# Kernel optimization log

Measured on AMD Instinct MI355X. Metric: run time of the kernel, lower is better.

Reference implementation:

```python
import jax, jax.numpy as jnp
import numpy as np

EMBED = 512
HEADS = 64
DK = EMBED // HEADS  # == n_wires_attn == 8
NW_FFN = 8
FFN = 2048
EPS = 1e-5


def _layernorm(x, g, b):
    mu = jnp.mean(x, axis=-1, keepdims=True)
    var = jnp.var(x, axis=-1, keepdims=True)
    return (x - mu) * jax.lax.rsqrt(var + EPS) * g + b


def setup_inputs() -> dict:
    key = jax.random.key(0)
    ks = jax.random.split(key, 12)
    d = {
        "x": jax.random.normal(ks[0], (4, 1024, EMBED), dtype=jnp.float32),
        # attention quantum RX params (one per wire, shared across heads/tokens)
        "phi": jax.random.normal(ks[1], (DK,), dtype=jnp.float32) * 0.1,
        # combine_heads linear
        "Wc": jax.random.normal(ks[2], (EMBED, EMBED), dtype=jnp.float32) / np.sqrt(EMBED),
        "bc": jnp.zeros((EMBED,), dtype=jnp.float32),
        # FFN quantum RY params
        "theta": jax.random.normal(ks[3], (NW_FFN,), dtype=jnp.float32) * 0.1,
        "W1": jax.random.normal(ks[4], (NW_FFN, FFN), dtype=jnp.float32) / np.sqrt(NW_FFN),
        "b1": jnp.zeros((FFN,), dtype=jnp.float32),
        "W2": jax.random.normal(ks[5], (FFN, EMBED), dtype=jnp.float32) / np.sqrt(FFN),
        "b2": jnp.zeros((EMBED,), dtype=jnp.float32),
        "g1": jnp.ones((EMBED,), dtype=jnp.float32),
        "be1": jnp.zeros((EMBED,), dtype=jnp.float32),
        "g2": jnp.ones((EMBED,), dtype=jnp.float32),
        "be2": jnp.zeros((EMBED,), dtype=jnp.float32),
    }
    return d


def reference(x, phi, Wc, bc, theta, W1, b1, W2, b2, g1, be1, g2, be2):
    B, S, E = x.shape
    # --- quantum attention projections ---
    # Per head-row of DK features: RX(x_i) encoder then trainable RX(phi_i),
    xh = x.reshape(B, S, HEADS, DK)
    qkv = jnp.cos(xh + phi)                     # [B,S,H,DK]
    qkv = jnp.transpose(qkv, (0, 2, 1, 3))      # [B,H,S,DK]
    scores = jnp.einsum('bhqd,bhkd->bhqk', qkv, qkv) / jnp.sqrt(jnp.float32(DK))
    attn = jax.nn.softmax(scores, axis=-1)
    out = jnp.einsum('bhqk,bhkd->bhqd', attn, qkv)
    out = jnp.transpose(out, (0, 2, 1, 3)).reshape(B, S, E)
    attn_out = out @ Wc.T if False else out @ Wc + bc  # combine_heads linear
    x1 = _layernorm(x + attn_out, g1, be1)
    # --- quantum FFN: RX(x_i) then trainable RY(theta_i) -> <Z> = cos(x_i)*cos(theta_i)
    qout = jnp.cos(x1[..., :NW_FFN]) * jnp.cos(theta)   # [B,S,NW_FFN]
    h = jax.nn.relu(qout @ W1 + b1)
    ffn_out = h @ W2 + b2
    return _layernorm(x1 + ffn_out, g2, be2)
```

## Files before the change

kernel.cpp:

```cpp
#include <hip/hip_runtime.h>
#include <hip/hip_bf16.h>
#include <math.h>

#define B 4
#define S 1024
#define E 512
#define H 64
#define DK 8
#define FFN 2048
#define BS (B*S)

#define CSCALE 0.7141879f

#if __has_builtin(__builtin_amdgcn_exp2f)
#define EXP2F(x) __builtin_amdgcn_exp2f(x)
#else
#define EXP2F(x) exp2f(x)
#endif

typedef __attribute__((ext_vector_type(8))) short short8;
typedef __attribute__((ext_vector_type(4))) float float4a;

union U8 { short8 v; unsigned u[4]; };
union F4 { float4a v; float f[4]; };

__device__ __forceinline__ unsigned short f2bf(float f) {
    unsigned u = __builtin_bit_cast(unsigned, f);
    u = (u + 0x7fffu + ((u >> 16) & 1u)) >> 16;
    return (unsigned short)u;
}
__device__ __forceinline__ float bf2f(unsigned short h) {
    return __builtin_bit_cast(float, (unsigned)h << 16);
}
__device__ __forceinline__ unsigned packbf(float a, float b) {
    return __builtin_amdgcn_perm(__builtin_bit_cast(unsigned, a),
                                 __builtin_bit_cast(unsigned, b), 0x07060302u);
}
__device__ __forceinline__ unsigned packbf_rn(float a, float b) {
    return ((unsigned)f2bf(a) << 16) | f2bf(b);
}
__device__ __forceinline__ int pidx(int k) {
    return (k & ~31) | (((k >> 2) & 3) << 3) | (((k >> 4) & 1) << 2) | (k & 3);
}

__device__ __forceinline__ void glds16(const void* g, void* l) {
    __builtin_amdgcn_global_load_lds(
        (const __attribute__((address_space(1))) void*)g,
        (__attribute__((address_space(3))) void*)l, 16, 0, 0);
}

__global__ __launch_bounds__(512) void attn_conv_kernel(const float* __restrict__ x,
                                                        const float* __restrict__ phi,
                                                        const float* __restrict__ Wc,
                                                        const float* __restrict__ W2,
                                                        const float* __restrict__ W1,
                                                        const float* __restrict__ b1,
                                                        unsigned short* __restrict__ Afrag,
                                                        unsigned short* __restrict__ W2f,
                                                        unsigned short* __restrict__ Wcf,
                                                        unsigned short* __restrict__ W1f) {
    __shared__ unsigned short kv[(S + 16) * DK];
    __shared__ unsigned short vtp[9][S + 8];
    int bid = blockIdx.x;
    int tid = threadIdx.x;
    const short8 z8 = {0,0,0,0,0,0,0,0};

    if (bid < 336) {
        int idx = bid * 512 + tid;
        if (idx < 131072) {
            int lane = idx & 63, c = idx >> 6;
            int ntile = c >> 6, kb32 = c & 63;
            int g = lane >> 4, col = lane & 15;
            int n = ntile * 16 + col, kb = kb32 * 32;
            short8 o;
            #pragma unroll
            for (int j = 0; j < 8; j++) {
                int k = kb + 16 * (j >> 2) + 4 * g + (j & 3);
                o[j] = (short)f2bf(W2[(size_t)k * 512 + n]);
            }
            *(short8*)&W2f[(size_t)idx * 8] = o;
        } else if (idx < 163840) {
            int i2 = idx - 131072;
            int lane = i2 & 63, c = i2 >> 6;
            int ntile = c >> 4, kb32 = c & 15;
            int g = lane >> 4, col = lane & 15;
            int n = ntile * 16 + col, kb = kb32 * 32;
            short8 o;
            #pragma unroll
            for (int j = 0; j < 8; j++)
                o[j] = (short)f2bf(Wc[(size_t)(kb + g * 8 + j) * 512 + n]);
            *(short8*)&Wcf[(size_t)i2 * 8] = o;
        } else {
            int i3 = idx - 163840;
            if (i3 < 2048) {
                short8 o;
                #pragma unroll
                for (int j = 0; j < 8; j++) o[j] = (short)f2bf(W1[j * FFN + i3]);
                *(short8*)&W1f[(size_t)i3 * 8] = o;
            } else if (i3 < 4096) {
                int f = i3 - 2048;
                short8 o = z8;
                o[0] = (short)f2bf(b1[f]);
                *(short8*)&W1f[(size_t)i3 * 8] = o;
            } else if (i3 < 4112) {
                *(short8*)&W1f[(size_t)i3 * 8] = z8;
            }
        }
        return;
    }

    int abid = bid - 336;
    int head = abid >> 2, qquad = abid & 3;
    int b = head >> 6, hh = head & 63;

    float ph[DK];
    #pragma unroll
    for (int d = 0; d < DK; d++) ph[d] = phi[d];

    {
        int r2 = tid * 2;
        unsigned short vb[8][2];
        #pragma unroll
        for (int j = 0; j < 2; j++) {
            const float* xp = x + ((size_t)(b * S + r2 + j)) * E + hh * DK;
            float4 u = *(const float4*)xp;
            float4 v = *(const float4*)(xp + 4);
            float c[8] = {__cosf(u.x+ph[0]), __cosf(u.y+ph[1]), __cosf(u.z+ph[2]), __cosf(u.w+ph[3]),
                          __cosf(v.x+ph[4]), __cosf(v.y+ph[5]), __cosf(v.z+ph[6]), __cosf(v.w+ph[7])};
            U8 kr;
            kr.u[0] = packbf_rn(c[1] * CSCALE, c[0] * CSCALE);
            kr.u[1] = packbf_rn(c[3] * CSCALE, c[2] * CSCALE);
            kr.u[2] = packbf_rn(c[5] * CSCALE, c[4] * CSCALE);
            kr.u[3] = packbf_rn(c[7] * CSCALE, c[6] * CSCALE);
            *(short8*)&kv[(r2 + j) * DK] = kr.v;
            #pragma unroll
            for (int d = 0; d < 8; d++) vb[d][j] = f2bf(c[d]);
        }
        int pr = pidx(r2);
        #pragma unroll
        for (int d = 0; d < 8; d++)
            *(unsigned*)&vtp[d][pr] = (unsigned)vb[d][0] | ((unsigned)vb[d][1] << 16);
        *(unsigned*)&vtp[8][pr] = 0x3F803F80u;
    }
    if (tid < 16) *(short8*)&kv[(S + tid) * DK] = z8;
    __syncthreads();

    int w = tid >> 6, lane = tid & 63, col = lane & 15, g = lane >> 4;
    bool g0 = (g == 0);
    int q0 = qquad * 256 + w * 32;
    const float4a zc = {0.f,0.f,0.f,0.f};

    short8 aq[2];
    #pragma unroll
    for (int t = 0; t < 2; t++)
        aq[t] = g0 ? *(const short8*)&kv[(q0 + t*16 + col) * DK] : z8;

    float4a acc[2];
    acc[0] = zc; acc[1] = zc;

    int vrow = col < 8 ? col : 8;
    const unsigned short* vbase = &vtp[vrow][0];

    int off0 = g0 ? col * DK : S * DK;
    int off1 = g0 ? (16 + col) * DK : S * DK;
    int stepo = g0 ? 32 * DK : 0;

    short8 bk0 = *(const short8*)&kv[off0];
    short8 bk1 = *(const short8*)&kv[off1];
    off0 += stepo; off1 += stepo;
    short8 bkN0 = *(const short8*)&kv[off0];
    short8 bkN1 = *(const short8*)&kv[off1];
    off0 += stepo; off1 += stepo;
    float4a s00 = __builtin_amdgcn_mfma_f32_16x16x32_bf16(bk0, aq[0], zc, 0,0,0);
    float4a s01 = __builtin_amdgcn_mfma_f32_16x16x32_bf16(bk1, aq[0], zc, 0,0,0);
    float4a s10 = __builtin_amdgcn_mfma_f32_16x16x32_bf16(bk0, aq[1], zc, 0,0,0);
    float4a s11 = __builtin_amdgcn_mfma_f32_16x16x32_bf16(bk1, aq[1], zc, 0,0,0);
    short8 vf = *(const short8*)(vbase + g * 8);

#define EXP_PACK(PF0, PF1)                                                      \
        F4 S00, S01, S10, S11;                                                  \
        S00.v = s00; S01.v = s01; S10.v = s10; S11.v = s11;                     \
        float ea0 = EXP2F(S00.f[0]);                                            \
        float ea1 = EXP2F(S00.f[1]);                                            \
        float ea2 = EXP2F(S00.f[2]);                                            \
        float ea3 = EXP2F(S00.f[3]);                                            \
        float eb0 = EXP2F(S01.f[0]);                                            \
        float eb1 = EXP2F(S01.f[1]);                                            \
        float eb2 = EXP2F(S01.f[2]);                                            \
        float eb3 = EXP2F(S01.f[3]);                                            \
        float ec0 = EXP2F(S10.f[0]);                                            \
        float ec1 = EXP2F(S10.f[1]);                                            \
        float ec2 = EXP2F(S10.f[2]);                                            \
        float ec3 = EXP2F(S10.f[3]);                                            \
        float ed0 = EXP2F(S11.f[0]);                                            \
        float ed1 = EXP2F(S11.f[1]);                                            \
        float ed2 = EXP2F(S11.f[2]);                                            \
        float ed3 = EXP2F(S11.f[3]);                                            \
        PF0.u[0] = packbf(ea1, ea0);                                            \
        PF0.u[1] = packbf(ea3, ea2);                                            \
        PF0.u[2] = packbf(eb1, eb0);                                            \
        PF0.u[3] = packbf(eb3, eb2);                                            \
        PF1.u[0] = packbf(ec1, ec0);                                            \
        PF1.u[1] = packbf(ec3, ec2);                                            \
        PF1.u[2] = packbf(ed1, ed0);                                            \
        PF1.u[3] = packbf(ed3, ed2);

    for (int kb = 0; kb < S - 32; kb += 32) {
        short8 nb0 = *(const short8*)&kv[off0];
        short8 nb1 = *(const short8*)&kv[off1];
        off0 += stepo; off1 += stepo;
        short8 vfN = *(const short8*)(vbase + kb + 32 + g * 8);
        U8 pf0, pf1;
        { EXP_PACK(pf0, pf1) }
        float4a t00 = __builtin_amdgcn_mfma_f32_16x16x32_bf16(bkN0, aq[0], zc, 0,0,0);
        float4a t01 = __builtin_amdgcn_mfma_f32_16x16x32_bf16(bkN1, aq[0], zc, 0,0,0);
        float4a t10 = __builtin_amdgcn_mfma_f32_16x16x32_bf16(bkN0, aq[1], zc, 0,0,0);
        float4a t11 = __builtin_amdgcn_mfma_f32_16x16x32_bf16(bkN1, aq[1], zc, 0,0,0);
        acc[0] = __builtin_amdgcn_mfma_f32_16x16x32_bf16(vf, pf0.v, acc[0], 0,0,0);
        acc[1] = __builtin_amdgcn_mfma_f32_16x16x32_bf16(vf, pf1.v, acc[1], 0,0,0);
        s00 = t00; s01 = t01; s10 = t10; s11 = t11;
        bkN0 = nb0; bkN1 = nb1; vf = vfN;
    }
    {
        U8 pf0, pf1;
        { EXP_PACK(pf0, pf1) }
        acc[0] = __builtin_amdgcn_mfma_f32_16x16x32_bf16(vf, pf0.v, acc[0], 0,0,0);
        acc[1] = __builtin_amdgcn_mfma_f32_16x16x32_bf16(vf, pf1.v, acc[1], 0,0,0);
    }
#undef EXP_PACK

    int lp8 = ((hh & 3) * 16 + col) * 8;
    #pragma unroll
    for (int t = 0; t < 2; t++) {
        F4 a; a.v = acc[t];
        float denom = __shfl(a.f[0], 32 + col);
        float inv = __builtin_amdgcn_rcpf(denom);
        if (g < 2) {
            int chunk = (hh >> 2) * 256 + (b * 64 + qquad * 16 + w * 2 + t);
            uint2 o;
            o.x = packbf_rn(a.f[1] * inv, a.f[0] * inv);
            o.y = packbf_rn(a.f[3] * inv, a.f[2] * inv);
            *(uint2*)&Afrag[(size_t)chunk * 512 + lp8 + g * 4] = o;
        }
    }
}

__global__ __launch_bounds__(512) void combine_ln1(const unsigned short* __restrict__ Afrag,
                                                   const unsigned short* __restrict__ Wcf,
                                                   const float* __restrict__ bc,
                                                   const float* __restrict__ x,
                                                   const float* __restrict__ g1,
                                                   const float* __restrict__ be1,
                                                   float* __restrict__ x1out,
                                                   unsigned short* __restrict__ qoutbf,
                                                   const float* __restrict__ theta) {
    __shared__ unsigned short As[16 * 64 * 8];
    __shared__ float xout[16][516];
    int tt = blockIdx.x;
    int tid = threadIdx.x;
    int w = tid >> 6, lane = tid & 63;
    int wbase = (tid & ~63) * 8;

    #pragma unroll
    for (int r = 0; r < 2; r++) {
        const unsigned short* gsrc =
            Afrag + ((size_t)((r * 8 + w) * 256 + tt) * 64 + lane) * 8;
        glds16(gsrc, &As[r * 4096 + wbase]);
    }
    asm volatile("s_waitcnt vmcnt(0)" ::: "memory");
    __syncthreads();

    int col = lane & 15, g = lane >> 4;
    const float4a zc = {0.f,0.f,0.f,0.f};
    float4a acc[4];
    #pragma unroll
    for (int nt = 0; nt < 4; nt++) acc[nt] = zc;

    const unsigned short* wp = Wcf + ((size_t)(w * 4096) + lane) * 8;

    short8 bfA[4], bfB[4];
    #pragma unroll
    for (int nt = 0; nt < 4; nt++)
        bfA[nt] = *(const short8*)(wp + nt * 8192);

    for (int kb32 = 0; kb32 < 16; kb32 += 2) {
        #pragma unroll
        for (int nt = 0; nt < 4; nt++)
            bfB[nt] = *(const short8*)(wp + nt * 8192 + (kb32 + 1) * 512);
        short8 af = *(const short8*)&As[(kb32 * 64 + lane) * 8];
        #pragma unroll
        for (int nt = 0; nt < 4; nt++)
            acc[nt] = __builtin_amdgcn_mfma_f32_16x16x32_bf16(af, bfA[nt], acc[nt], 0, 0, 0);
        if (kb32 + 2 < 16) {
            #pragma unroll
            for (int nt = 0; nt < 4; nt++)
                bfA[nt] = *(const short8*)(wp + nt * 8192 + (kb32 + 2) * 512);
        }
        af = *(const short8*)&As[((kb32 + 1) * 64 + lane) * 8];
        #pragma unroll
        for (int nt = 0; nt < 4; nt++)
            acc[nt] = __builtin_amdgcn_mfma_f32_16x16x32_bf16(af, bfB[nt], acc[nt], 0, 0, 0);
    }
    #pragma unroll
    for (int nt = 0; nt < 4; nt++) {
        int n = w * 64 + nt * 16 + col;
        float bb = bc[n];
        #pragma unroll
        for (int r = 0; r < 4; r++)
            xout[g * 4 + r][n] = acc[nt][r] + bb;
    }
    __syncthreads();

    int hl = lane >> 5, l = lane & 31;
    int token = w * 2 + hl;
    int e0 = l * 16;
    size_t grow = ((size_t)tt * 16 + token) * 512;
    float v[16];
    float s = 0.f, sq = 0.f;
    #pragma unroll
    for (int u = 0; u < 4; u++) {
        float4 xv = *(const float4*)&x[grow + e0 + u * 4];
        float4 pv = *(const float4*)&xout[token][e0 + u * 4];
        float a0 = xv.x + pv.x, a1 = xv.y + pv.y, a2 = xv.z + pv.z, a3 = xv.w + pv.w;
        v[u*4] = a0; v[u*4+1] = a1; v[u*4+2] = a2; v[u*4+3] = a3;
        s += a0 + a1 + a2 + a3;
        sq += a0*a0 + a1*a1 + a2*a2 + a3*a3;
    }
    #pragma unroll
    for (int off = 1; off <= 16; off <<= 1) {
        s  += __shfl_xor(s, off);
        sq += __shfl_xor(sq, off);
    }
    float mu = s * (1.f / 512.f);
    float var = sq * (1.f / 512.f) - mu * mu;
    float rstd = rsqrtf(var + 1e-5f);
    float y[16];
    #pragma unroll
    for (int u = 0; u < 4; u++) {
        float4 gv = *(const float4*)&g1[e0 + u * 4];
        float4 bv = *(const float4*)&be1[e0 + u * 4];
        y[u*4]   = (v[u*4]   - mu) * rstd * gv.x + bv.x;
        y[u*4+1] = (v[u*4+1] - mu) * rstd * gv.y + bv.y;
        y[u*4+2] = (v[u*4+2] - mu) * rstd * gv.z + bv.z;
        y[u*4+3] = (v[u*4+3] - mu) * rstd * gv.w + bv.w;
        float4 o = make_float4(y[u*4], y[u*4+1], y[u*4+2], y[u*4+3]);
        *(float4*)&x1out[grow + e0 + u * 4] = o;
    }
    if (l == 0) {
        U8 q;
        q.u[0] = packbf_rn(__cosf(y[1]) * __cosf(theta[1]), __cosf(y[0]) * __cosf(theta[0]));
        q.u[1] = packbf_rn(__cosf(y[3]) * __cosf(theta[3]), __cosf(y[2]) * __cosf(theta[2]));
        q.u[2] = packbf_rn(__cosf(y[5]) * __cosf(theta[5]), __cosf(y[4]) * __cosf(theta[4]));
        q.u[3] = packbf_rn(__cosf(y[7]) * __cosf(theta[7]), __cosf(y[6]) * __cosf(theta[6]));
        *(short8*)&qoutbf[((size_t)tt * 16 + token) * 8] = q.v;
    }
}

__global__ __launch_bounds__(256) void ffn_mfma(const unsigned short* __restrict__ qbf,
                                                const unsigned short* __restrict__ W1fg,
                                                const unsigned short* __restrict__ W2f,
                                                const float* __restrict__ b2,
                                                unsigned short* __restrict__ Cbf) {
    __shared__ float accs[2][64][36];
    int tid = threadIdx.x;
    int w = tid >> 6, lane = tid & 63, col = lane & 15, g = lane >> 4;
    int ngw = w & 1, kh = w >> 1;
    int tb = blockIdx.x >> 2, nb = blockIdx.x & 3;
    int mw = tb * 32;
    int ntile0 = nb * 8 + ngw * 4;
    int kb32b = kh * 32;
    const short8 z8 = {0,0,0,0,0,0,0,0};
    const short8 one8 = {(short)0x3F80,0,0,0,0,0,0,0};
    const float4a zc = {0.f,0.f,0.f,0.f};

    short8 qf[2];
    #pragma unroll
    for (int t = 0; t < 2; t++)
        qf[t] = (g == 0) ? *(const short8*)&qbf[(size_t)(mw + t * 16 + col) * 8]
                         : (g == 1 ? one8 : z8);

    float4a acc[2][4];
    #pragma unroll
    for (int t = 0; t < 2; t++)
        #pragma unroll
        for (int nt = 0; nt < 4; nt++) acc[t][nt] = zc;

    const unsigned short* w2p = W2f + (size_t)ntile0 * 64 * 512 + lane * 8;
    const unsigned short* w1p =
        (g == 0) ? W1fg + (size_t)(kb32b * 32 + col) * 8 :
        (g == 1) ? W1fg + 16384 + (size_t)(kb32b * 32 + col) * 8 :
                   W1fg + 32768;
    int w1step = (g < 2) ? 256 : 0;

    short8 afA[4], afB[4], w1A0, w1A1, w1B0, w1B1;
    #pragma unroll
    for (int nt = 0; nt < 4; nt++)
        afA[nt] = *(const short8*)(w2p + nt * 32768 + (size_t)kb32b * 512);
    w1A0 = *(const short8*)w1p;
    w1A1 = *(const short8*)(w1p + 128);
    w1p += w1step;

#define FFN_BODY(AF, W10, W11)                                                    \
    {                                                                             \
        _Pragma("unroll")                                                         \
        for (int t = 0; t < 2; t++) {                                             \
            float4a h0 = __builtin_amdgcn_mfma_f32_16x16x32_bf16(W10, qf[t], zc, 0,0,0); \
            float4a h1 = __builtin_amdgcn_mfma_f32_16x16x32_bf16(W11, qf[t], zc, 0,0,0); \
            F4 H0, H1; H0.v = h0; H1.v = h1;                                      \
            float e00 = fmaxf(H0.f[0], 0.f);                                      \
            float e01 = fmaxf(H0.f[1], 0.f);                                      \
            float e02 = fmaxf(H0.f[2], 0.f);                                      \
            float e03 = fmaxf(H0.f[3], 0.f);                                      \
            float e10 = fmaxf(H1.f[0], 0.f);                                      \
            float e11 = fmaxf(H1.f[1], 0.f);                                      \
            float e12 = fmaxf(H1.f[2], 0.f);                                      \
            float e13 = fmaxf(H1.f[3], 0.f);                                      \
            U8 pf;                                                                \
            pf.u[0] = packbf(e01, e00);                                           \
            pf.u[1] = packbf(e03, e02);                                           \
            pf.u[2] = packbf(e11, e10);                                           \
            pf.u[3] = packbf(e13, e12);                                           \
            _Pragma("unroll")                                                     \
            for (int nt = 0; nt < 4; nt++)                                        \
                acc[t][nt] = __builtin_amdgcn_mfma_f32_16x16x32_bf16(AF[nt], pf.v, \
                                                                     acc[t][nt], 0,0,0); \
        }                                                                         \
    }

    for (int i = 0; i < 32; i += 2) {
        int kb32 = kb32b + i;
        #pragma unroll
        for (int nt = 0; nt < 4; nt++)
            afB[nt] = *(const short8*)(w2p + nt * 32768 + (size_t)(kb32 + 1) * 512);
        w1B0 = *(const short8*)w1p;
        w1B1 = *(const short8*)(w1p + 128);
        w1p += w1step;
        FFN_BODY(afA, w1A0, w1A1)
        #pragma unroll
        for (int nt = 0; nt < 4; nt++)
            afA[nt] = *(const short8*)(w2p + nt * 32768 + (size_t)(kb32 + 2) * 512);
        w1A0 = *(const short8*)w1p;
        w1A1 = *(const short8*)(w1p + 128);
        w1p += w1step;
        FFN_BODY(afB, w1B0, w1B1)
    }
#undef FFN_BODY

    if (kh == 1) {
        #pragma unroll
        for (int t = 0; t < 2; t++)
            #pragma unroll
            for (int nt = 0; nt < 4; nt++)
                *(float4a*)&accs[ngw][lane][(t * 4 + nt) * 4] = acc[t][nt];
    }
    __syncthreads();
    if (kh == 0) {
        #pragma unroll
        for (int t = 0; t < 2; t++)
            #pragma unroll
            for (int nt = 0; nt < 4; nt++)
                acc[t][nt] = acc[t][nt] +
                    *(const float4a*)&accs[ngw][lane][(t * 4 + nt) * 4];
        int n0 = ntile0 * 16;
        #pragma unroll
        for (int nt = 0; nt < 4; nt++) {
            float4 bb = *(const float4*)&b2[n0 + nt * 16 + 4 * g];
            #pragma unroll
            for (int t = 0; t < 2; t++) {
                F4 a; a.v = acc[t][nt];
                uint2 o;
                o.x = packbf_rn(a.f[1] + bb.y, a.f[0] + bb.x);
                o.y = packbf_rn(a.f[3] + bb.w, a.f[2] + bb.z);
                *(uint2*)&Cbf[(size_t)(mw + t * 16 + col) * 512 + n0 + nt * 16 + 4 * g] = o;
            }
        }
    }
}

__global__ __launch_bounds__(256) void ln_kernel(const float* __restrict__ a,
                                                 const unsigned short* __restrict__ r,
                                                 const float* __restrict__ g,
                                                 const float* __restrict__ be,
                                                 float* __restrict__ out) {
    int t = blockIdx.x * 4 + (threadIdx.x >> 6);
    int lane = threadIdx.x & 63;
    size_t base = (size_t)t * E;
    int e0 = lane * 8;
    float4 a0 = *(const float4*)&a[base + e0];
    float4 a1 = *(const float4*)&a[base + e0 + 4];
    uint4 rv = *(const uint4*)&r[base + e0];
    float v[8];
    v[0] = a0.x + bf2f((unsigned short)(rv.x & 0xffff));
    v[1] = a0.y + bf2f((unsigned short)(rv.x >> 16));
    v[2] = a0.z + bf2f((unsigned short)(rv.y & 0xffff));
    v[3] = a0.w + bf2f((unsigned short)(rv.y >> 16));
    v[4] = a1.x + bf2f((unsigned short)(rv.z & 0xffff));
    v[5] = a1.y + bf2f((unsigned short)(rv.z >> 16));
    v[6] = a1.z + bf2f((unsigned short)(rv.w & 0xffff));
    v[7] = a1.w + bf2f((unsigned short)(rv.w >> 16));
    float s = 0.f, sq = 0.f;
    #pragma unroll
    for (int i = 0; i < 8; i++) { s += v[i]; sq += v[i] * v[i]; }
    #pragma unroll
    for (int off = 1; off <= 32; off <<= 1) {
        s  += __shfl_xor(s, off);
        sq += __shfl_xor(sq, off);
    }
    float mu = s * (1.f / E);
    float var = sq * (1.f / E) - mu * mu;
    float rstd = rsqrtf(var + 1e-5f);
    float4 g0 = *(const float4*)&g[e0];
    float4 g1v = *(const float4*)&g[e0 + 4];
    float4 b0 = *(const float4*)&be[e0];
    float4 b1v = *(const float4*)&be[e0 + 4];
    float4 o0, o1;
    o0.x = (v[0] - mu) * rstd * g0.x + b0.x;
    o0.y = (v[1] - mu) * rstd * g0.y + b0.y;
    o0.z = (v[2] - mu) * rstd * g0.z + b0.z;
    o0.w = (v[3] - mu) * rstd * g0.w + b0.w;
    o1.x = (v[4] - mu) * rstd * g1v.x + b1v.x;
    o1.y = (v[5] - mu) * rstd * g1v.y + b1v.y;
    o1.z = (v[6] - mu) * rstd * g1v.z + b1v.z;
    o1.w = (v[7] - mu) * rstd * g1v.w + b1v.w;
    *(float4*)&out[base + e0] = o0;
    *(float4*)&out[base + e0 + 4] = o1;
}

extern "C" void kernel_launch(void* const* d_in, const int* in_sizes, int n_in,
                              void* d_out, int out_size, void* d_ws, size_t ws_size,
                              hipStream_t stream) {
    const float* x     = (const float*)d_in[0];
    const float* phi   = (const float*)d_in[1];
    const float* Wc    = (const float*)d_in[2];
    const float* bc    = (const float*)d_in[3];
    const float* theta = (const float*)d_in[4];
    const float* W1    = (const float*)d_in[5];
    const float* b1    = (const float*)d_in[6];
    const float* W2    = (const float*)d_in[7];
    const float* b2    = (const float*)d_in[8];
    const float* g1    = (const float*)d_in[9];
    const float* be1   = (const float*)d_in[10];
    const float* g2    = (const float*)d_in[11];
    const float* be2   = (const float*)d_in[12];
    float* out = (float*)d_out;

    float* ws = (float*)d_ws;
    unsigned short* Afrag  = (unsigned short*)ws;
    unsigned short* W2f    = (unsigned short*)(ws + 1048576);
    unsigned short* Wcf    = (unsigned short*)(ws + 1572864);
    unsigned short* W1f    = (unsigned short*)(ws + 1703936);
    unsigned short* qoutbf = (unsigned short*)(ws + 1736704);

    attn_conv_kernel<<<1360, 512, 0, stream>>>(x, phi, Wc, W2, W1, b1,
                                               Afrag, W2f, Wcf, W1f);
    combine_ln1<<<256, 512, 0, stream>>>(Afrag, Wcf, bc, x, g1, be1,
                                         out, qoutbf, theta);
    ffn_mfma<<<512, 256, 0, stream>>>(qoutbf, W1f, W2f, b2, Afrag);
    ln_kernel<<<1024, 256, 0, stream>>>(out, Afrag, g2, be2, out);
}
```

Measured before the change: 156.9 us.

## Fuse combine, FFN and final layernorm into one persistent kernel with grid barriers

Merges the combine+LN1, FFN MFMA and LN2 kernels into a single 256-block kernel that uses a software grid barrier (atomic counter plus generation) between phases. The aim is to drop two kernel launches and their launch gaps. The counter is reset by the first kernel. The barrier relies on all 256 blocks being co-resident, and the FFN phase now runs with 256 blocks of 512 threads in place of 512 blocks of 256. The FFN output buffer Cbf aliases Afrag, which phase one reads; this is safe only because the grid barrier orders the two phases.

```diff
diff --git a/kernel.cpp b/kernel.cpp
--- a/kernel.cpp
+++ b/kernel.cpp
@@ -47,6 +47,25 @@
     __builtin_amdgcn_global_load_lds(
         (const __attribute__((address_space(1))) void*)g,
         (__attribute__((address_space(3))) void*)l, 16, 0, 0);
+}
+
+__device__ __forceinline__ void gridbar(unsigned* cnt, unsigned* gen) {
+    __syncthreads();
+    __threadfence();
+    if (threadIdx.x == 0) {
+        unsigned g = __hip_atomic_load(gen, __ATOMIC_RELAXED, __HIP_MEMORY_SCOPE_AGENT);
+        unsigned old = __hip_atomic_fetch_add(cnt, 1u, __ATOMIC_ACQ_REL,
+                                              __HIP_MEMORY_SCOPE_AGENT);
+        if (old == 255u) {
+            __hip_atomic_store(cnt, 0u, __ATOMIC_RELAXED, __HIP_MEMORY_SCOPE_AGENT);
+            __hip_atomic_store(gen, g + 1u, __ATOMIC_RELEASE, __HIP_MEMORY_SCOPE_AGENT);
+        } else {
+            while (__hip_atomic_load(gen, __ATOMIC_ACQUIRE,
+                                     __HIP_MEMORY_SCOPE_AGENT) == g)
+                __builtin_amdgcn_s_sleep(2);
+        }
+    }
+    __syncthreads();
 }
 
 __global__ __launch_bounds__(512) void attn_conv_kernel(const float* __restrict__ x,
@@ -58,7 +77,8 @@
                                                         unsigned short* __restrict__ Afrag,
                                                         unsigned short* __restrict__ W2f,
                                                         unsigned short* __restrict__ Wcf,
-                                                        unsigned short* __restrict__ W1f) {
+                                                        unsigned short* __restrict__ W1f,
+                                                        unsigned* __restrict__ bar) {
     __shared__ unsigned short kv[(S + 16) * DK];
     __shared__ unsigned short vtp[9][S + 8];
     int bid = blockIdx.x;
@@ -67,6 +87,7 @@
 
     if (bid < 336) {
         int idx = bid * 512 + tid;
+        if (idx == 0) { bar[0] = 0u; bar[1] = 0u; }
         if (idx < 131072) {
             int lane = idx & 63, c = idx >> 6;
             int ntile = c >> 6, kb32 = c & 63;
@@ -245,285 +266,290 @@
     }
 }
 
-__global__ __launch_bounds__(512) void combine_ln1(const unsigned short* __restrict__ Afrag,
-                                                   const unsigned short* __restrict__ Wcf,
-                                                   const float* __restrict__ bc,
-                                                   const float* __restrict__ x,
-                                                   const float* __restrict__ g1,
-                                                   const float* __restrict__ be1,
-                                                   float* __restrict__ x1out,
-                                                   unsigned short* __restrict__ qoutbf,
-                                                   const float* __restrict__ theta) {
-    __shared__ unsigned short As[16 * 64 * 8];
-    __shared__ float xout[16][516];
-    int tt = blockIdx.x;
-    int tid = threadIdx.x;
-    int w = tid >> 6, lane = tid & 63;
-    int wbase = (tid & ~63) * 8;
-
-    #pragma unroll
-    for (int r = 0; r < 2; r++) {
-        const unsigned short* gsrc =
-            Afrag + ((size_t)((r * 8 + w) * 256 + tt) * 64 + lane) * 8;
-        glds16(gsrc, &As[r * 4096 + wbase]);
-    }
-    asm volatile("s_waitcnt vmcnt(0)" ::: "memory");
-    __syncthreads();
-
-    int col = lane & 15, g = lane >> 4;
-    const float4a zc = {0.f,0.f,0.f,0.f};
-    float4a acc[4];
-    #pragma unroll
-    for (int nt = 0; nt < 4; nt++) acc[nt] = zc;
-
-    const unsigned short* wp = Wcf + ((size_t)(w * 4096) + lane) * 8;
-
-    short8 bfA[4], bfB[4];
-    #pragma unroll
-    for (int nt = 0; nt < 4; nt++)
-        bfA[nt] = *(const short8*)(wp + nt * 8192);
-
-    for (int kb32 = 0; kb32 < 16; kb32 += 2) {
-        #pragma unroll
-        for (int nt = 0; nt < 4; nt++)
-            bfB[nt] = *(const short8*)(wp + nt * 8192 + (kb32 + 1) * 512);
-        short8 af = *(const short8*)&As[(kb32 * 64 + lane) * 8];
-        #pragma unroll
-        for (int nt = 0; nt < 4; nt++)
-            acc[nt] = __builtin_amdgcn_mfma_f32_16x16x32_bf16(af, bfA[nt], acc[nt], 0, 0, 0);
-        if (kb32 + 2 < 16) {
-            #pragma unroll
-            for (int nt = 0; nt < 4; nt++)
-                bfA[nt] = *(const short8*)(wp + nt * 8192 + (kb32 + 2) * 512);
-        }
-        af = *(const short8*)&As[((kb32 + 1) * 64 + lane) * 8];
-        #pragma unroll
-        for (int nt = 0; nt < 4; nt++)
-            acc[nt] = __builtin_amdgcn_mfma_f32_16x16x32_bf16(af, bfB[nt], acc[nt], 0, 0, 0);
-    }
-    #pragma unroll
-    for (int nt = 0; nt < 4; nt++) {
-        int n = w * 64 + nt * 16 + col;
-        float bb = bc[n];
-        #pragma unroll
-        for (int r = 0; r < 4; r++)
-            xout[g * 4 + r][n] = acc[nt][r] + bb;
-    }
-    __syncthreads();
-
-    int hl = lane >> 5, l = lane & 31;
-    int token = w * 2 + hl;
-    int e0 = l * 16;
-    size_t grow = ((size_t)tt * 16 + token) * 512;
-    float v[16];
-    float s = 0.f, sq = 0.f;
-    #pragma unroll
-    for (int u = 0; u < 4; u++) {
-        float4 xv = *(const float4*)&x[grow + e0 + u * 4];
-        float4 pv = *(const float4*)&xout[token][e0 + u * 4];
-        float a0 = xv.x + pv.x, a1 = xv.y + pv.y, a2 = xv.z + pv.z, a3 = xv.w + pv.w;
-        v[u*4] = a0; v[u*4+1] = a1; v[u*4+2] = a2; v[u*4+3] = a3;
-        s += a0 + a1 + a2 + a3;
-        sq += a0*a0 + a1*a1 + a2*a2 + a3*a3;
-    }
-    #pragma unroll
-    for (int off = 1; off <= 16; off <<= 1) {
-        s  += __shfl_xor(s, off);
-        sq += __shfl_xor(sq, off);
-    }
-    float mu = s * (1.f / 512.f);
-    float var = sq * (1.f / 512.f) - mu * mu;
-    float rstd = rsqrtf(var + 1e-5f);
-    float y[16];
-    #pragma unroll
-    for (int u = 0; u < 4; u++) {
-        float4 gv = *(const float4*)&g1[e0 + u * 4];
-        float4 bv = *(const float4*)&be1[e0 + u * 4];
-        y[u*4]   = (v[u*4]   - mu) * rstd * gv.x + bv.x;
-        y[u*4+1] = (v[u*4+1] - mu) * rstd * gv.y + bv.y;
-        y[u*4+2] = (v[u*4+2] - mu) * rstd * gv.z + bv.z;
-        y[u*4+3] = (v[u*4+3] - mu) * rstd * gv.w + bv.w;
-        float4 o = make_float4(y[u*4], y[u*4+1], y[u*4+2], y[u*4+3]);
-        *(float4*)&x1out[grow + e0 + u * 4] = o;
-    }
-    if (l == 0) {
-        U8 q;
-        q.u[0] = packbf_rn(__cosf(y[1]) * __cosf(theta[1]), __cosf(y[0]) * __cosf(theta[0]));
-        q.u[1] = packbf_rn(__cosf(y[3]) * __cosf(theta[3]), __cosf(y[2]) * __cosf(theta[2]));
-        q.u[2] = packbf_rn(__cosf(y[5]) * __cosf(theta[5]), __cosf(y[4]) * __cosf(theta[4]));
-        q.u[3] = packbf_rn(__cosf(y[7]) * __cosf(theta[7]), __cosf(y[6]) * __cosf(theta[6]));
-        *(short8*)&qoutbf[((size_t)tt * 16 + token) * 8] = q.v;
-    }
-}
-
-__global__ __launch_bounds__(256) void ffn_mfma(const unsigned short* __restrict__ qbf,
-                                                const unsigned short* __restrict__ W1fg,
-                                                const unsigned short* __restrict__ W2f,
-                                                const float* __restrict__ b2,
-                                                unsigned short* __restrict__ Cbf) {
-    __shared__ float accs[2][64][36];
+__global__ __launch_bounds__(512) void fused_tail(const unsigned short* __restrict__ Afrag,
+                                                  const unsigned short* __restrict__ Wcf,
+                                                  const float* __restrict__ bc,
+                                                  const float* __restrict__ x,
+                                                  const float* __restrict__ g1,
+                                                  const float* __restrict__ be1,
+                                                  const float* __restrict__ theta,
+                                                  const unsigned short* __restrict__ W1fg,
+                                                  const unsigned short* __restrict__ W2f,
+                                                  const float* __restrict__ b2,
+                                                  const float* __restrict__ g2,
+                                                  const float* __restrict__ be2,
+                                                  unsigned short* __restrict__ qoutbf,
+                                                  float* __restrict__ out,
+                                                  unsigned short* __restrict__ Cbf,
+                                                  unsigned* __restrict__ bar) {
+    __shared__ union {
+        struct { unsigned short As[16 * 64 * 8]; float xout[16][516]; } a;
+        struct { float accs[2][2][64][36]; } b3;
+    } sm;
+    int bid = blockIdx.x;
     int tid = threadIdx.x;
     int w = tid >> 6, lane = tid & 63, col = lane & 15, g = lane >> 4;
-    int ngw = w & 1, kh = w >> 1;
-    int tb = blockIdx.x >> 2, nb = blockIdx.x & 3;
-    int mw = tb * 32;
-    int ntile0 = nb * 8 + ngw * 4;
-    int kb32b = kh * 32;
+    const float4a zc = {0.f,0.f,0.f,0.f};
     const short8 z8 = {0,0,0,0,0,0,0,0};
-    const short8 one8 = {(short)0x3F80,0,0,0,0,0,0,0};
-    const float4a zc = {0.f,0.f,0.f,0.f};
-
-    short8 qf[2];
-    #pragma unroll
-    for (int t = 0; t < 2; t++)
-        qf[t] = (g == 0) ? *(const short8*)&qbf[(size_t)(mw + t * 16 + col) * 8]
-                         : (g == 1 ? one8 : z8);
-
-    float4a acc[2][4];
-    #pragma unroll
-    for (int t = 0; t < 2; t++)
-        #pragma unroll
-        for (int nt = 0; nt < 4; nt++) acc[t][nt] = zc;
-
-    const unsigned short* w2p = W2f + (size_t)ntile0 * 64 * 512 + lane * 8;
-    const unsigned short* w1p =
-        (g == 0) ? W1fg + (size_t)(kb32b * 32 + col) * 8 :
-        (g == 1) ? W1fg + 16384 + (size_t)(kb32b * 32 + col) * 8 :
-                   W1fg + 32768;
-    int w1step = (g < 2) ? 256 : 0;
-
-    short8 afA[4], afB[4], w1A0, w1A1, w1B0, w1B1;
-    #pragma unroll
-    for (int nt = 0; nt < 4; nt++)
-        afA[nt] = *(const short8*)(w2p + nt * 32768 + (size_t)kb32b * 512);
-    w1A0 = *(const short8*)w1p;
-    w1A1 = *(const short8*)(w1p + 128);
-    w1p += w1step;
-
-#define FFN_BODY(AF, W10, W11)                                                    \
-    {                                                                             \
-        _Pragma("unroll")                                                         \
-        for (int t = 0; t < 2; t++) {                                             \
-            float4a h0 = __builtin_amdgcn_mfma_f32_16x16x32_bf16(W10, qf[t], zc, 0,0,0); \
-            float4a h1 = __builtin_amdgcn_mfma_f32_16x16x32_bf16(W11, qf[t], zc, 0,0,0); \
-            F4 H0, H1; H0.v = h0; H1.v = h1;                                      \
-            float e00 = fmaxf(H0.f[0], 0.f);                                      \
-            float e01 = fmaxf(H0.f[1], 0.f);                                      \
-            float e02 = fmaxf(H0.f[2], 0.f);                                      \
-            float e03 = fmaxf(H0.f[3], 0.f);                                      \
-            float e10 = fmaxf(H1.f[0], 0.f);                                      \
-            float e11 = fmaxf(H1.f[1], 0.f);                                      \
-            float e12 = fmaxf(H1.f[2], 0.f);                                      \
-            float e13 = fmaxf(H1.f[3], 0.f);                                      \
-            U8 pf;                                                                \
-            pf.u[0] = packbf(e01, e00);                                           \
-            pf.u[1] = packbf(e03, e02);                                           \
-            pf.u[2] = packbf(e11, e10);                                           \
-            pf.u[3] = packbf(e13, e12);                                           \
-            _Pragma("unroll")                                                     \
-            for (int nt = 0; nt < 4; nt++)                                        \
-                acc[t][nt] = __builtin_amdgcn_mfma_f32_16x16x32_bf16(AF[nt], pf.v, \
-                                                                     acc[t][nt], 0,0,0); \
-        }                                                                         \
-    }
-
-    for (int i = 0; i < 32; i += 2) {
-        int kb32 = kb32b + i;
+
+    {
+        int tt = bid;
+        int wbase = (tid & ~63) * 8;
+        #pragma unroll
+        for (int r = 0; r < 2; r++) {
+            const unsigned short* gsrc =
+                Afrag + ((size_t)((r * 8 + w) * 256 + tt) * 64 + lane) * 8;
+            glds16(gsrc, &sm.a.As[r * 4096 + wbase]);
+        }
+        asm volatile("s_waitcnt vmcnt(0)" ::: "memory");
+        __syncthreads();
+
+        float4a acc[4];
+        #pragma unroll
+        for (int nt = 0; nt < 4; nt++) acc[nt] = zc;
+
+        const unsigned short* wp = Wcf + ((size_t)(w * 4096) + lane) * 8;
+
+        short8 bfA[4], bfB[4];
         #pragma unroll
         for (int nt = 0; nt < 4; nt++)
-            afB[nt] = *(const short8*)(w2p + nt * 32768 + (size_t)(kb32 + 1) * 512);
-        w1B0 = *(const short8*)w1p;
-        w1B1 = *(const short8*)(w1p + 128);
-        w1p += w1step;
-        FFN_BODY(afA, w1A0, w1A1)
+            bfA[nt] = *(const short8*)(wp + nt * 8192);
+
+        for (int kb32 = 0; kb32 < 16; kb32 += 2) {
+            #pragma unroll
+            for (int nt = 0; nt < 4; nt++)
+                bfB[nt] = *(const short8*)(wp + nt * 8192 + (kb32 + 1) * 512);
+            short8 af = *(const short8*)&sm.a.As[(kb32 * 64 + lane) * 8];
+            #pragma unroll
+            for (int nt = 0; nt < 4; nt++)
+                acc[nt] = __builtin_amdgcn_mfma_f32_16x16x32_bf16(af, bfA[nt], acc[nt], 0, 0, 0);
+            if (kb32 + 2 < 16) {
+                #pragma unroll
+                for (int nt = 0; nt < 4; nt++)
+                    bfA[nt] = *(const short8*)(wp + nt * 8192 + (kb32 + 2) * 512);
+            }
+            af = *(const short8*)&sm.a.As[((kb32 + 1) * 64 + lane) * 8];
+            #pragma unroll
+            for (int nt = 0; nt < 4; nt++)
+                acc[nt] = __builtin_amdgcn_mfma_f32_16x16x32_bf16(af, bfB[nt], acc[nt], 0, 0, 0);
+        }
+        #pragma unroll
+        for (int nt = 0; nt < 4; nt++) {
+            int n = w * 64 + nt * 16 + col;
+            float bb = bc[n];
+            #pragma unroll
+            for (int r = 0; r < 4; r++)
+                sm.a.xout[g * 4 + r][n] = acc[nt][r] + bb;
+        }
+        __syncthreads();
+
+        int hl = lane >> 5, l = lane & 31;
+        int token = w * 2 + hl;
+        int e0 = l * 16;
+        size_t grow = ((size_t)tt * 16 + token) * 512;
+        float v[16];
+        float s = 0.f, sq = 0.f;
+        #pragma unroll
+        for (int u = 0; u < 4; u++) {
+            float4 xv = *(const float4*)&x[grow + e0 + u * 4];
+            float4 pv = *(const float4*)&sm.a.xout[token][e0 + u * 4];
+            float a0 = xv.x + pv.x, a1 = xv.y + pv.y, a2 = xv.z + pv.z, a3 = xv.w + pv.w;
+            v[u*4] = a0; v[u*4+1] = a1; v[u*4+2] = a2; v[u*4+3] = a3;
+            s += a0 + a1 + a2 + a3;
+            sq += a0*a0 + a1*a1 + a2*a2 + a3*a3;
+        }
+        #pragma unroll
+        for (int off = 1; off <= 16; off <<= 1) {
+            s  += __shfl_xor(s, off);
+            sq += __shfl_xor(sq, off);
+        }
+        float mu = s * (1.f / 512.f);
+        float var = sq * (1.f / 512.f) - mu * mu;
+        float rstd = rsqrtf(var + 1e-5f);
+        float y[16];
+        #pragma unroll
+        for (int u = 0; u < 4; u++) {
+            float4 gv = *(const float4*)&g1[e0 + u * 4];
+            float4 bv = *(const float4*)&be1[e0 + u * 4];
+            y[u*4]   = (v[u*4]   - mu) * rstd * gv.x + bv.x;
+            y[u*4+1] = (v[u*4+1] - mu) * rstd * gv.y + bv.y;
+            y[u*4+2] = (v[u*4+2] - mu) * rstd * gv.z + bv.z;
+            y[u*4+3] = (v[u*4+3] - mu) * rstd * gv.w + bv.w;
+            float4 o = make_float4(y[u*4], y[u*4+1], y[u*4+2], y[u*4+3]);
+            *(float4*)&out[grow + e0 + u * 4] = o;
+        }
+        if (l == 0) {
+            U8 q;
+            q.u[0] = packbf_rn(__cosf(y[1]) * __cosf(theta[1]), __cosf(y[0]) * __cosf(theta[0]));
+            q.u[1] = packbf_rn(__cosf(y[3]) * __cosf(theta[3]), __cosf(y[2]) * __cosf(theta[2]));
+            q.u[2] = packbf_rn(__cosf(y[5]) * __cosf(theta[5]), __cosf(y[4]) * __cosf(theta[4]));
+            q.u[3] = packbf_rn(__cosf(y[7]) * __cosf(theta[7]), __cosf(y[6]) * __cosf(theta[6]));
+            *(short8*)&qoutbf[((size_t)tt * 16 + token) * 8] = q.v;
+        }
+    }
+
+    gridbar(&bar[0], &bar[1]);
+
+    {
+        int sub = w >> 2, lw = w & 3;
+        int fbid = bid * 2 + sub;
+        int ngw = lw & 1, kh = lw >> 1;
+        int tb = fbid >> 2, nb3 = fbid & 3;
+        int mw = tb * 32;
+        int ntile0 = nb3 * 8 + ngw * 4;
+        int kb32b = kh * 32;
+        const short8 one8 = {(short)0x3F80,0,0,0,0,0,0,0};
+
+        short8 qf[2];
+        #pragma unroll
+        for (int t = 0; t < 2; t++)
+            qf[t] = (g == 0) ? *(const short8*)&qoutbf[(size_t)(mw + t * 16 + col) * 8]
+                             : (g == 1 ? one8 : z8);
+
+        float4a acc[2][4];
+        #pragma unroll
+        for (int t = 0; t < 2; t++)
+            #pragma unroll
+            for (int nt = 0; nt < 4; nt++) acc[t][nt] = zc;
+
+        const unsigned short* w2p = W2f + (size_t)ntile0 * 64 * 512 + lane * 8;
+        const unsigned short* w1p =
+            (g == 0) ? W1fg + (size_t)(kb32b * 32 + col) * 8 :
+            (g == 1) ? W1fg + 16384 + (size_t)(kb32b * 32 + col) * 8 :
+                       W1fg + 32768;
+        int w1step = (g < 2) ? 256 : 0;
+
+        short8 afA[4], afB[4], w1A0, w1A1, w1B0, w1B1;
         #pragma unroll
         for (int nt = 0; nt < 4; nt++)
-            afA[nt] = *(const short8*)(w2p + nt * 32768 + (size_t)(kb32 + 2) * 512);
+            afA[nt] = *(const short8*)(w2p + nt * 32768 + (size_t)kb32b * 512);
         w1A0 = *(const short8*)w1p;
         w1A1 = *(const short8*)(w1p + 128);
         w1p += w1step;
-        FFN_BODY(afB, w1B0, w1B1)
-    }
+
+#define FFN_BODY(AF, W10, W11)                                                    \
+        {                                                                         \
+            _Pragma("unroll")                                                     \
+            for (int t = 0; t < 2; t++) {                                         \
+                float4a h0 = __builtin_amdgcn_mfma_f32_16x16x32_bf16(W10, qf[t], zc, 0,0,0); \
+                float4a h1 = __builtin_amdgcn_mfma_f32_16x16x32_bf16(W11, qf[t], zc, 0,0,0); \
+                F4 H0, H1; H0.v = h0; H1.v = h1;                                  \
+                float e00 = fmaxf(H0.f[0], 0.f);                                  \
+                float e01 = fmaxf(H0.f[1], 0.f);                                  \
+                float e02 = fmaxf(H0.f[2], 0.f);                                  \
+                float e03 = fmaxf(H0.f[3], 0.f);                                  \
+                float e10 = fmaxf(H1.f[0], 0.f);                                  \
+                float e11 = fmaxf(H1.f[1], 0.f);                                  \
+                float e12 = fmaxf(H1.f[2], 0.f);                                  \
+                float e13 = fmaxf(H1.f[3], 0.f);                                  \
+                U8 pf;                                                            \
+                pf.u[0] = packbf(e01, e00);                                       \
+                pf.u[1] = packbf(e03, e02);                                       \
+                pf.u[2] = packbf(e11, e10);                                       \
+                pf.u[3] = packbf(e13, e12);                                       \
+                _Pragma("unroll")                                                 \
+                for (int nt = 0; nt < 4; nt++)                                    \
+                    acc[t][nt] = __builtin_amdgcn_mfma_f32_16x16x32_bf16(AF[nt], pf.v, \
+                                                                         acc[t][nt], 0,0,0); \
+            }                                                                     \
+        }
+
+        for (int i = 0; i < 32; i += 2) {
+            int kb32 = kb32b + i;
+            #pragma unroll
+            for (int nt = 0; nt < 4; nt++)
+                afB[nt] = *(const short8*)(w2p + nt * 32768 + (size_t)(kb32 + 1) * 512);
+            w1B0 = *(const short8*)w1p;
+            w1B1 = *(const short8*)(w1p + 128);
+            w1p += w1step;
+            FFN_BODY(afA, w1A0, w1A1)
+            #pragma unroll
+            for (int nt = 0; nt < 4; nt++)
+                afA[nt] = *(const short8*)(w2p + nt * 32768 + (size_t)(kb32 + 2) * 512);
+            w1A0 = *(const short8*)w1p;
+            w1A1 = *(const short8*)(w1p + 128);
+            w1p += w1step;
+            FFN_BODY(afB, w1B0, w1B1)
+        }
 #undef FFN_BODY
 
-    if (kh == 1) {
-        #pragma unroll
-        for (int t = 0; t < 2; t++)
-            #pragma unroll
-            for (int nt = 0; nt < 4; nt++)
-                *(float4a*)&accs[ngw][lane][(t * 4 + nt) * 4] = acc[t][nt];
-    }
-    __syncthreads();
-    if (kh == 0) {
-        #pragma unroll
-        for (int t = 0; t < 2; t++)
-            #pragma unroll
-            for (int nt = 0; nt < 4; nt++)
-                acc[t][nt] = acc[t][nt] +
-                    *(const float4a*)&accs[ngw][lane][(t * 4 + nt) * 4];
-        int n0 = ntile0 * 16;
-        #pragma unroll
-        for (int nt = 0; nt < 4; nt++) {
-            float4 bb = *(const float4*)&b2[n0 + nt * 16 + 4 * g];
-            #pragma unroll
-            for (int t = 0; t < 2; t++) {
-                F4 a; a.v = acc[t][nt];
-                uint2 o;
-                o.x = packbf_rn(a.f[1] + bb.y, a.f[0] + bb.x);
-                o.y = packbf_rn(a.f[3] + bb.w, a.f[2] + bb.z);
-                *(uint2*)&Cbf[(size_t)(mw + t * 16 + col) * 512 + n0 + nt * 16 + 4 * g] = o;
+        if (kh == 1) {
+            #pragma unroll
+            for (int t = 0; t < 2; t++)
+                #pragma unroll
+                for (int nt = 0; nt < 4; nt++)
+                    *(float4a*)&sm.b3.accs[sub][ngw][lane][(t * 4 + nt) * 4] = acc[t][nt];
+        }
+        __syncthreads();
+        if (kh == 0) {
+            #pragma unroll
+            for (int t = 0; t < 2; t++)
+                #pragma unroll
+                for (int nt = 0; nt < 4; nt++)
+                    acc[t][nt] = acc[t][nt] +
+                        *(const float4a*)&sm.b3.accs[sub][ngw][lane][(t * 4 + nt) * 4];
+            int n0 = ntile0 * 16;
+            #pragma unroll
+            for (int nt = 0; nt < 4; nt++) {
+                float4 bb = *(const float4*)&b2[n0 + nt * 16 + 4 * g];
+                #pragma unroll
+                for (int t = 0; t < 2; t++) {
+                    F4 a; a.v = acc[t][nt];
+                    uint2 o;
+                    o.x = packbf_rn(a.f[1] + bb.y, a.f[0] + bb.x);
+                    o.y = packbf_rn(a.f[3] + bb.w, a.f[2] + bb.z);
+                    *(uint2*)&Cbf[(size_t)(mw + t * 16 + col) * 512 + n0 + nt * 16 + 4 * g] = o;
+                }
             }
         }
     }
-}
-
-__global__ __launch_bounds__(256) void ln_kernel(const float* __restrict__ a,
-                                                 const unsigned short* __restrict__ r,
-                                                 const float* __restrict__ g,
-                                                 const float* __restrict__ be,
-                                                 float* __restrict__ out) {
-    int t = blockIdx.x * 4 + (threadIdx.x >> 6);
-    int lane = threadIdx.x & 63;
-    size_t base = (size_t)t * E;
-    int e0 = lane * 8;
-    float4 a0 = *(const float4*)&a[base + e0];
-    float4 a1 = *(const float4*)&a[base + e0 + 4];
-    uint4 rv = *(const uint4*)&r[base + e0];
-    float v[8];
-    v[0] = a0.x + bf2f((unsigned short)(rv.x & 0xffff));
-    v[1] = a0.y + bf2f((unsigned short)(rv.x >> 16));
-    v[2] = a0.z + bf2f((unsigned short)(rv.y & 0xffff));
-    v[3] = a0.w + bf2f((unsigned short)(rv.y >> 16));
-    v[4] = a1.x + bf2f((unsigned short)(rv.z & 0xffff));
-    v[5] = a1.y + bf2f((unsigned short)(rv.z >> 16));
-    v[6] = a1.z + bf2f((unsigned short)(rv.w & 0xffff));
-    v[7] = a1.w + bf2f((unsigned short)(rv.w >> 16));
-    float s = 0.f, sq = 0.f;
+
+    gridbar(&bar[0], &bar[1]);
+
     #pragma unroll
-    for (int i = 0; i < 8; i++) { s += v[i]; sq += v[i] * v[i]; }
-    #pragma unroll
-    for (int off = 1; off <= 32; off <<= 1) {
-        s  += __shfl_xor(s, off);
-        sq += __shfl_xor(sq, off);
-    }
-    float mu = s * (1.f / E);
-    float var = sq * (1.f / E) - mu * mu;
-    float rstd = rsqrtf(var + 1e-5f);
-    float4 g0 = *(const float4*)&g[e0];
-    float4 g1v = *(const float4*)&g[e0 + 4];
-    float4 b0 = *(const float4*)&be[e0];
-    float4 b1v = *(const float4*)&be[e0 + 4];
-    float4 o0, o1;
-    o0.x = (v[0] - mu) * rstd * g0.x + b0.x;
-    o0.y = (v[1] - mu) * rstd * g0.y + b0.y;
-    o0.z = (v[2] - mu) * rstd * g0.z + b0.z;
-    o0.w = (v[3] - mu) * rstd * g0.w + b0.w;
-    o1.x = (v[4] - mu) * rstd * g1v.x + b1v.x;
-    o1.y = (v[5] - mu) * rstd * g1v.y + b1v.y;
-    o1.z = (v[6] - mu) * rstd * g1v.z + b1v.z;
-    o1.w = (v[7] - mu) * rstd * g1v.w + b1v.w;
-    *(float4*)&out[base + e0] = o0;
-    *(float4*)&out[base + e0 + 4] = o1;
+    for (int it = 0; it < 2; it++) {
+        int t = bid * 16 + it * 8 + w;
+        size_t base = (size_t)t * E;
+        int e0 = lane * 8;
+        float4 a0 = *(const float4*)&out[base + e0];
+        float4 a1 = *(const float4*)&out[base + e0 + 4];
+        uint4 rv = *(const uint4*)&Cbf[base + e0];
+        float v[8];
+        v[0] = a0.x + bf2f((unsigned short)(rv.x & 0xffff));
+        v[1] = a0.y + bf2f((unsigned short)(rv.x >> 16));
+        v[2] = a0.z + bf2f((unsigned short)(rv.y & 0xffff));
+        v[3] = a0.w + bf2f((unsigned short)(rv.y >> 16));
+        v[4] = a1.x + bf2f((unsigned short)(rv.z & 0xffff));
+        v[5] = a1.y + bf2f((unsigned short)(rv.z >> 16));
+        v[6] = a1.z + bf2f((unsigned short)(rv.w & 0xffff));
+        v[7] = a1.w + bf2f((unsigned short)(rv.w >> 16));
+        float s = 0.f, sq = 0.f;
+        #pragma unroll
+        for (int i = 0; i < 8; i++) { s += v[i]; sq += v[i] * v[i]; }
+        #pragma unroll
+        for (int off = 1; off <= 32; off <<= 1) {
+            s  += __shfl_xor(s, off);
+            sq += __shfl_xor(sq, off);
+        }
+        float mu = s * (1.f / E);
+        float var = sq * (1.f / E) - mu * mu;
+        float rstd = rsqrtf(var + 1e-5f);
+        float4 g0v = *(const float4*)&g2[e0];
+        float4 g1v = *(const float4*)&g2[e0 + 4];
+        float4 b0v = *(const float4*)&be2[e0];
+        float4 b1v = *(const float4*)&be2[e0 + 4];
+        float4 o0, o1;
+        o0.x = (v[0] - mu) * rstd * g0v.x + b0v.x;
+        o0.y = (v[1] - mu) * rstd * g0v.y + b0v.y;
+        o0.z = (v[2] - mu) * rstd * g0v.z + b0v.z;
+        o0.w = (v[3] - mu) * rstd * g0v.w + b0v.w;
+        o1.x = (v[4] - mu) * rstd * g1v.x + b1v.x;
+        o1.y = (v[5] - mu) * rstd * g1v.y + b1v.y;
+        o1.z = (v[6] - mu) * rstd * g1v.z + b1v.z;
+        o1.w = (v[7] - mu) * rstd * g1v.w + b1v.w;
+        *(float4*)&out[base + e0] = o0;
+        *(float4*)&out[base + e0 + 4] = o1;
+    }
 }
 
 extern "C" void kernel_launch(void* const* d_in, const int* in_sizes, int n_in,
@@ -550,11 +576,11 @@
     unsigned short* Wcf    = (unsigned short*)(ws + 1572864);
     unsigned short* W1f    = (unsigned short*)(ws + 1703936);
     unsigned short* qoutbf = (unsigned short*)(ws + 1736704);
+    unsigned* bar          = (unsigned*)(ws + 1753088);
 
     attn_conv_kernel<<<1360, 512, 0, stream>>>(x, phi, Wc, W2, W1, b1,
-                                               Afrag, W2f, Wcf, W1f);
-    combine_ln1<<<256, 512, 0, stream>>>(Afrag, Wcf, bc, x, g1, be1,
-                                         out, qoutbf, theta);
-    ffn_mfma<<<512, 256, 0, stream>>>(qoutbf, W1f, W2f, b2, Afrag);
-    ln_kernel<<<1024, 256, 0, stream>>>(out, Afrag, g2, be2, out);
-}
+                                               Afrag, W2f, Wcf, W1f, bar);
+    fused_tail<<<256, 512, 0, stream>>>(Afrag, Wcf, bc, x, g1, be1, theta,
+                                        W1f, W2f, b2, g2, be2,
+                                        qoutbf, out, Afrag, bar);
+}
```

Result: slower. 281.8 us (+79.6%).
